# Optimization experiments

Hardware: AMD Instinct MI355X
Metric: run time of the kernel (lower is better)

The kernel has to match this reference:

```python
import jax, jax.numpy as jnp
import numpy as np

R = 32  # voxel resolution
B, CIN, COUT, N = 4, 64, 64, 4096
K = 3


def setup_inputs():
    key = jax.random.key(0)
    ks = jax.random.split(key, 8)
    s = 0.05
    return {
        "features": jax.random.normal(ks[0], (B, CIN, N), jnp.float32),
        "coords": jax.random.normal(ks[1], (B, 3, N), jnp.float32),
        # voxel branch: conv3d + BN x2
        "w1": jax.random.normal(ks[2], (COUT, CIN, K, K, K), jnp.float32) * s,
        "b1": jnp.zeros((COUT,), jnp.float32),
        "g1": jnp.ones((COUT,), jnp.float32),
        "be1": jnp.zeros((COUT,), jnp.float32),
        "w2": jax.random.normal(ks[3], (COUT, COUT, K, K, K), jnp.float32) * s,
        "b2": jnp.zeros((COUT,), jnp.float32),
        "g2": jnp.ones((COUT,), jnp.float32),
        "be2": jnp.zeros((COUT,), jnp.float32),
        # point branch SharedMLP (1x1 conv + BN + ReLU)
        "wp": jax.random.normal(ks[4], (COUT, CIN), jnp.float32) * s,
        "bp": jnp.zeros((COUT,), jnp.float32),
        "gp": jnp.ones((COUT,), jnp.float32),
        "bep": jnp.zeros((COUT,), jnp.float32),
        # fuzzy_proj 1x1 conv
        "wf": jax.random.normal(ks[5], (COUT, CIN), jnp.float32) * s,
        "bf": jnp.zeros((COUT,), jnp.float32),
        # fusion SharedMLP (3*COUT -> COUT)
        "wfu": jax.random.normal(ks[6], (COUT, 3 * COUT), jnp.float32) * s,
        "bfu": jnp.zeros((COUT,), jnp.float32),
        "gfu": jnp.ones((COUT,), jnp.float32),
        "befu": jnp.zeros((COUT,), jnp.float32),
    }


def _bn3d(x, g, b):
    # training-mode BatchNorm3d, eps=1e-4 (biased variance, as torch)
    m = x.mean((0, 2, 3, 4), keepdims=True)
    v = x.var((0, 2, 3, 4), keepdims=True)
    return (x - m) * jax.lax.rsqrt(v + 1e-4) * g[None, :, None, None, None] + b[None, :, None, None, None]


def _bn1d(x, g, b):
    m = x.mean((0, 2), keepdims=True)
    v = x.var((0, 2), keepdims=True)
    return (x - m) * jax.lax.rsqrt(v + 1e-4) * g[None, :, None] + b[None, :, None]


def _conv3d(x, w, b):
    pad = K // 2
    y = jax.lax.conv_general_dilated(x, w, (1, 1, 1), [(pad, pad)] * 3,
                                     dimension_numbers=('NCDHW', 'OIDHW', 'NCDHW'))
    return y + b[None, :, None, None, None]


def _conv1x1(x, w, b):
    return jnp.einsum('oc,bcn->bon', w, x) + b[None, :, None]


def _voxelize(features, coords):
    # PVCNN Voxelization(normalize=True, eps=0): center, scale to unit, grid coords in [0, R-1]
    nc = coords - coords.mean(axis=2, keepdims=True)              # [B,3,N]
    norm = jnp.linalg.norm(nc, axis=1, keepdims=True)             # [B,1,N]
    nc = nc / (norm.max(axis=2, keepdims=True) * 2.0) + 0.5
    nc = jnp.clip(nc * R, 0.0, R - 1)
    vox = jnp.round(nc).astype(jnp.int32)                         # [B,3,N]
    b_, c_, n_ = features.shape
    idx = (vox[:, 0] * R + vox[:, 1]) * R + vox[:, 2]             # [B,N]
    flat = (idx + jnp.arange(b_)[:, None] * R ** 3).reshape(-1)
    feat = features.transpose(0, 2, 1).reshape(b_ * n_, c_)
    sums = jax.ops.segment_sum(feat, flat, num_segments=b_ * R ** 3)
    cnt = jax.ops.segment_sum(jnp.ones((b_ * n_,), feat.dtype), flat, num_segments=b_ * R ** 3)
    avg = sums / jnp.maximum(cnt, 1.0)[:, None]                   # scatter-mean
    grid = avg.reshape(b_, R ** 3, c_).transpose(0, 2, 1).reshape(b_, c_, R, R, R)
    return grid, nc


def _devoxelize(grid, nc):
    # trilinear gather: grid [B,C,R,R,R], nc [B,3,N] float coords in [0,R-1]
    b_, c_ = grid.shape[:2]
    g = grid.reshape(b_, c_, -1)
    lo_f = jnp.floor(nc)
    fr = nc - lo_f                                                # fractional part [B,3,N]
    lo = lo_f.astype(jnp.int32)
    hi = jnp.minimum(lo + 1, R - 1)
    out = jnp.zeros((b_, c_, nc.shape[2]), grid.dtype)
    for dx in (0, 1):
        for dy in (0, 1):
            for dz in (0, 1):
                ix = hi[:, 0] if dx else lo[:, 0]
                iy = hi[:, 1] if dy else lo[:, 1]
                iz = hi[:, 2] if dz else lo[:, 2]
                w = ((fr[:, 0] if dx else 1.0 - fr[:, 0]) *
                     (fr[:, 1] if dy else 1.0 - fr[:, 1]) *
                     (fr[:, 2] if dz else 1.0 - fr[:, 2]))        # [B,N]
                flat = (ix * R + iy) * R + iz                     # [B,N]
                vals = jnp.take_along_axis(g, flat[:, None, :], axis=2)  # [B,C,N]
                out = out + vals * w[:, None, :]
    return out


def reference(features, coords, w1, b1, g1, be1, w2, b2, g2, be2,
              wp, bp, gp, bep, wf, bf, wfu, bfu, gfu, befu):
    lrelu = lambda x: jnp.where(x > 0, x, 0.1 * x)
    # voxel branch
    grid, nc = _voxelize(features, coords)
    v = lrelu(_bn3d(_conv3d(grid, w1, b1), g1, be1))
    v = lrelu(_bn3d(_conv3d(v, w2, b2), g2, be2))
    vox_feat = _devoxelize(v, nc)                                 # [B,COUT,N]
    # point branch
    pt = jax.nn.relu(_bn1d(_conv1x1(features, wp, bp), gp, bep))
    # fuzzy branch: dense attention over points
    cn = coords.transpose(0, 2, 1)                                # [B,N,3]
    cn = cn / jnp.maximum(jnp.linalg.norm(cn, axis=-1, keepdims=True), 1e-12)
    att = jax.nn.softmax(jnp.einsum('bnd,bmd->bnm', cn, cn) / 0.1, axis=-1)
    fz = jnp.einsum('bnm,bcm->bcn', att, features)                # [B,CIN,N]
    fz = _conv1x1(fz, wf, bf)
    # fusion
    comb = jnp.concatenate([vox_feat, pt, fz], axis=1)            # [B,3*COUT,N]
    fused = jax.nn.relu(_bn1d(_conv1x1(comb, wfu, bfu), gfu, befu))
    return (fused, coords)
```

## Files before the change

kernel.cpp:

```cpp
#include <hip/hip_runtime.h>
#include <hip/hip_bf16.h>
#include <math.h>

#define RR 32
#define R3 32768
#define BB 4
#define CI 64
#define CO 64
#define NN 4096

typedef short v8s __attribute__((ext_vector_type(8)));
typedef float v4f __attribute__((ext_vector_type(4)));
typedef unsigned short ushort_t;

__device__ __forceinline__ unsigned short f2bf(float f) {
    unsigned int u = __float_as_uint(f);
    unsigned int r = (u + 0x7FFFu + ((u >> 16) & 1u)) >> 16;
    return (unsigned short)r;
}

__device__ __forceinline__ void gll16(const void* g, void* l) {
    __builtin_amdgcn_global_load_lds((const __attribute__((address_space(1))) unsigned int*)g,
                                     (__attribute__((address_space(3))) unsigned int*)l, 16, 0, 0);
}

__device__ __forceinline__ float blockReduceSum(float v, float* sm) {
    int tid = threadIdx.x;
    sm[tid] = v; __syncthreads();
    for (int off = 128; off > 0; off >>= 1) {
        if (tid < off) sm[tid] += sm[tid + off];
        __syncthreads();
    }
    float r = sm[0]; __syncthreads();
    return r;
}
__device__ __forceinline__ float blockReduceMax(float v, float* sm) {
    int tid = threadIdx.x;
    sm[tid] = v; __syncthreads();
    for (int off = 128; off > 0; off >>= 1) {
        if (tid < off) sm[tid] = fmaxf(sm[tid], sm[tid + off]);
        __syncthreads();
    }
    float r = sm[0]; __syncthreads();
    return r;
}

__global__ void k_nc(const float* __restrict__ coords, float* __restrict__ nc,
                     int* __restrict__ vidx) {
    int b = blockIdx.x, tid = threadIdx.x;
    __shared__ float sm[256];
    const float* cb = coords + (size_t)b * 3 * NN;
    float s0 = 0, s1 = 0, s2 = 0;
    for (int n = tid; n < NN; n += 256) {
        s0 += cb[n]; s1 += cb[NN + n]; s2 += cb[2 * NN + n];
    }
    float m0 = blockReduceSum(s0, sm) * (1.0f / NN);
    float m1 = blockReduceSum(s1, sm) * (1.0f / NN);
    float m2 = blockReduceSum(s2, sm) * (1.0f / NN);
    float mx = 0;
    for (int n = tid; n < NN; n += 256) {
        float dx = cb[n] - m0, dy = cb[NN + n] - m1, dz = cb[2 * NN + n] - m2;
        mx = fmaxf(mx, dx * dx + dy * dy + dz * dz);
    }
    mx = blockReduceMax(mx, sm);
    float denom = 2.0f * sqrtf(mx);
    float mean[3] = {m0, m1, m2};
    for (int n = tid; n < NN; n += 256) {
        int vi[3];
        #pragma unroll
        for (int ax = 0; ax < 3; ax++) {
            float x = (cb[ax * NN + n] - mean[ax]) / denom + 0.5f;
            x = x * RR;
            x = fminf(fmaxf(x, 0.0f), (float)(RR - 1));
            nc[((size_t)b * 3 + ax) * NN + n] = x;
            vi[ax] = (int)rintf(x);
        }
        vidx[b * NN + n] = (vi[0] * RR + vi[1]) * RR + vi[2];
    }
}

__global__ void k_scatter(const float* __restrict__ feat, const int* __restrict__ vidx,
                          float* __restrict__ grid, float* __restrict__ cnt) {
    int i = blockIdx.x * 256 + threadIdx.x;
    int n = i & (NN - 1);
    int c = (i >> 12) & 63;
    int b = i >> 18;
    int idx = vidx[b * NN + n];
    atomicAdd(&grid[((size_t)(b * 64 + c)) * R3 + idx], feat[((size_t)(b * 64 + c)) * NN + n]);
    if (c == 0) atomicAdd(&cnt[b * R3 + idx], 1.0f);
}

__global__ void k_avgT(const float* __restrict__ grid, const float* __restrict__ cnt,
                       ushort_t* __restrict__ gT) {
    __shared__ float ld[64][65];
    int b = blockIdx.y, s0 = blockIdx.x * 64, tid = threadIdx.x;
    int sl = tid & 63, cq = tid >> 6;
    const float* xb = grid + (size_t)b * 64 * R3;
    #pragma unroll
    for (int k = 0; k < 16; k++) {
        int c = cq * 16 + k;
        ld[sl][c] = xb[(size_t)c * R3 + s0 + sl];
    }
    __syncthreads();
    int v = tid >> 2, q = tid & 3;
    float inv = 1.0f / fmaxf(cnt[b * R3 + s0 + v], 1.0f);
    unsigned int pk[8];
    #pragma unroll
    for (int j = 0; j < 8; j++) {
        int c = q * 16 + j * 2;
        float a = ld[v][c] * inv, d = ld[v][c + 1] * inv;
        pk[j] = (unsigned int)f2bf(a) | ((unsigned int)f2bf(d) << 16);
    }
    uint4* op = (uint4*)(gT + ((size_t)(b * R3 + s0 + v)) * 64 + q * 16);
    op[0] = make_uint4(pk[0], pk[1], pk[2], pk[3]);
    op[1] = make_uint4(pk[4], pk[5], pk[6], pk[7]);
}

__global__ void k_f2b(const float* __restrict__ x, ushort_t* __restrict__ o) {
    size_t i = (size_t)blockIdx.x * 256 + threadIdx.x;
    float4 a = ((const float4*)x)[i * 2];
    float4 b = ((const float4*)x)[i * 2 + 1];
    union { __hip_bfloat162 h[4]; uint4 u; } pk;
    pk.h[0] = __float22bfloat162_rn(make_float2(a.x, a.y));
    pk.h[1] = __float22bfloat162_rn(make_float2(a.z, a.w));
    pk.h[2] = __float22bfloat162_rn(make_float2(b.x, b.y));
    pk.h[3] = __float22bfloat162_rn(make_float2(b.z, b.w));
    ((uint4*)o)[i] = pk.u;
}

__global__ void k_tws(const float* __restrict__ w, ushort_t* __restrict__ wS) {
    int i = blockIdx.x * 256 + threadIdx.x;
    int cis = i & 31, co = (i >> 5) & 63;
    int dx = (i >> 11) % 3, cih = (i / 6144) & 1, dzdy = i / 12288;
    int k = dzdy * 3 + dx, ci = cih * 32 + cis;
    wS[i] = f2bf(w[((size_t)co * CI + ci) * 27 + k]);
}

__global__ void k_fold(const float* __restrict__ wp, const float* __restrict__ wfu,
                       const float* __restrict__ wf, const float* __restrict__ bf,
                       const float* __restrict__ bfu,
                       float* __restrict__ wpT, float* __restrict__ wfuT,
                       float* __restrict__ bC) {
    int i = blockIdx.x * 256 + threadIdx.x;
    if (i < 4096) {
        int c = i >> 6, o = i & 63;
        wpT[c * 64 + o] = wp[o * 64 + c];
    } else if (i < 12288) {
        int j = i - 4096;
        int c = j >> 6, o = j & 63;
        wfuT[c * 64 + o] = wfu[(size_t)o * 192 + c];
    } else if (i < 16384) {
        int j = i - 12288;
        int c = j >> 6, o = j & 63;
        float s = 0;
        for (int k = 0; k < 64; k++)
            s += wfu[(size_t)o * 192 + 128 + k] * wf[(size_t)k * 64 + c];
        wfuT[(128 + c) * 64 + o] = s;
    } else if (i < 16448) {
        int o = i - 16384;
        float s = bfu[o];
        for (int k = 0; k < 64; k++)
            s += wfu[(size_t)o * 192 + 128 + k] * bf[k];
        bC[o] = s;
    }
}

__global__ void k_bncast(const float* __restrict__ x, const float* __restrict__ accs,
                         const float* __restrict__ g, const float* __restrict__ be,
                         float invcnt, float slope, ushort_t* __restrict__ o) {
    size_t i = (size_t)blockIdx.x * 256 + threadIdx.x;
    int c0 = (int)((i * 8) & 63);
    float sc[8], sh[8];
    #pragma unroll
    for (int j = 0; j < 8; j++) {
        int c = c0 + j;
        float mean = accs[2 * c] * invcnt;
        float var = accs[2 * c + 1] * invcnt - mean * mean;
        float scale = g[c] * rsqrtf(var + 1e-4f);
        sc[j] = scale;
        sh[j] = be[c] - mean * scale;
    }
    float4 a = ((const float4*)x)[i * 2];
    float4 d = ((const float4*)x)[i * 2 + 1];
    float va[8] = {a.x, a.y, a.z, a.w, d.x, d.y, d.z, d.w};
    unsigned pk[4];
    #pragma unroll
    for (int j = 0; j < 4; j++) {
        float u0 = va[2 * j] * sc[2 * j] + sh[2 * j];
        float u1 = va[2 * j + 1] * sc[2 * j + 1] + sh[2 * j + 1];
        u0 = u0 > 0 ? u0 : slope * u0;
        u1 = u1 > 0 ? u1 : slope * u1;
        pk[j] = (unsigned)f2bf(u0) | ((unsigned)f2bf(u1) << 16);
    }
    ((uint4*)o)[i] = make_uint4(pk[0], pk[1], pk[2], pk[3]);
}

__global__ __launch_bounds__(256) void k_convlds(const ushort_t* __restrict__ gT,
                                                 const ushort_t* __restrict__ wS,
                                                 float* __restrict__ outCL,
                                                 float* __restrict__ accs) {
    __shared__ ushort_t lin[20480];
    __shared__ ushort_t lw[2][6144];
    int bid = blockIdx.x;
    int wgid = (bid & 7) * 64 + (bid >> 3);
    int yt = wgid & 3, z0 = (wgid >> 2) & 31, b = wgid >> 7;
    int tid = threadIdx.x;
    int w = __builtin_amdgcn_readfirstlane(tid >> 6);
    int lane = tid & 63, l15 = lane & 15, l4 = lane >> 4;
    int y0 = yt * 8;
    const ushort_t* gTb = gT + (size_t)b * R3 * 64;

    int voxF[4];
    #pragma unroll
    for (int f = 0; f < 4; f++)
        voxF[f] = (w * 2 + (f >> 1)) * 32 + (f & 1) * 16 + l15 - 1;
    bool xlo_ok = (l15 != 0), xhi_ok = (l15 != 15);

    const v8s vzero = {};
    v4f acc[4][4];
    #pragma unroll
    for (int m = 0; m < 4; m++)
        #pragma unroll
        for (int f = 0; f < 4; f++)
            acc[m][f] = (v4f){0.0f, 0.0f, 0.0f, 0.0f};

#define WSTAGE(s)                                                              \
    do {                                                                       \
        const ushort_t* _src = wS + (size_t)(s) * 6144;                        \
        ushort_t* _dst = lw[(s) & 1];                                          \
        _Pragma("unroll") for (int _i = 0; _i < 3; _i++) {                     \
            int _p = _i * 256 + w * 64;                                        \
            gll16(_src + (size_t)(_p + lane) * 8, _dst + (size_t)_p * 8);      \
        }                                                                      \
    } while (0)

#define ISTAGE(dz)                                                             \
    do {                                                                       \
        int _zp = z0 - 1 + (dz);                                               \
        if (_zp < 0 || _zp > 31) {                                             \
            for (int _q = 0; _q < 10; _q++)                                    \
                *(v8s*)&lin[(size_t)(w * 640 + _q * 64 + lane) * 8] = vzero;   \
        } else {                                                               \
            if (yt == 0) *(v8s*)&lin[(size_t)tid * 8] = vzero;                 \
            if (yt == 3) *(v8s*)&lin[(size_t)(2304 + tid) * 8] = vzero;        \
            const ushort_t* _pb = gTb + ((size_t)_zp * 1024 + (size_t)(y0 - 1) * 32) * 64; \
            int _g0 = (yt == 0) ? 256 : 0;                                     \
            int _nc = 10 - (yt == 0) - (yt == 3);                              \
            for (int _i = 0; _i < _nc; _i++) {                                 \
                int _pbase = _g0 + _i * 256 + w * 64;                          \
                int _p = _pbase + lane;                                        \
                int _vx = _p >> 3, _js = _p & 7;                               \
                int _sg = _vx * 8 + (_js ^ (_vx & 7));                         \
                gll16(_pb + (size_t)_sg * 8, lin + (size_t)_pbase * 8);        \
            }                                                                  \
        }                                                                      \
    } while (0)

    WSTAGE(0);
    for (int s = 0; s < 18; s++) {
        int dy = (s / 2) % 3, cih = s & 1;
        asm volatile("s_barrier" ::: "memory");
        if ((s % 6) == 0) ISTAGE(s / 6);
        if (s + 1 < 18) WSTAGE(s + 1);
        if (s + 1 < 18) asm volatile("s_waitcnt vmcnt(3) lgkmcnt(0)" ::: "memory");
        else            asm volatile("s_waitcnt vmcnt(0) lgkmcnt(0)" ::: "memory");
        asm volatile("s_barrier" ::: "memory");

        const ushort_t* lwb = lw[s & 1];
        #pragma unroll
        for (int dx = 0; dx < 3; dx++) {
            v8s Bf[4];
            #pragma unroll
            for (int f = 0; f < 4; f++) {
                int vox = voxF[f] + dy * 32 + dx;
                int g = vox * 8 + ((cih * 4 + l4) ^ (vox & 7));
                int bix = g * 16;
                bix = bix < 0 ? 0 : bix;
                v8s vb = *(const v8s*)((const char*)lin + bix);
                bool ok = (dx == 0 && (f & 1) == 0) ? xlo_ok :
                          (dx == 2 && (f & 1) == 1) ? xhi_ok : true;
                Bf[f] = ok ? vb : vzero;
            }
            const ushort_t* ap = lwb + dx * 2048 + l15 * 32 + l4 * 8;
            #pragma unroll
            for (int m = 0; m < 4; m++) {
                v8s Af = *(const v8s*)(ap + m * 512);
                #pragma unroll
                for (int f = 0; f < 4; f++)
                    acc[m][f] = __builtin_amdgcn_mfma_f32_16x16x32_bf16(Af, Bf[f], acc[m][f], 0, 0, 0);
            }
        }
    }

    #pragma unroll
    for (int m = 0; m < 4; m++) {
        #pragma unroll
        for (int f = 0; f < 4; f++) {
            int y = y0 + w * 2 + (f >> 1);
            int x = (f & 1) * 16 + l15;
            float4 o = make_float4(acc[m][f][0], acc[m][f][1], acc[m][f][2], acc[m][f][3]);
            *(float4*)&outCL[((size_t)b * R3 + z0 * 1024 + y * 32 + x) * 64 + m * 16 + l4 * 4] = o;
        }
    }

    __syncthreads();
    float* sbuf = (float*)lin;
    #pragma unroll
    for (int m = 0; m < 4; m++)
        #pragma unroll
        for (int r = 0; r < 4; r++) {
            float s = 0, q = 0;
            #pragma unroll
            for (int f = 0; f < 4; f++) {
                float v = acc[m][f][r];
                s += v; q += v * v;
            }
            sbuf[tid * 32 + (m * 4 + r) * 2] = s;
            sbuf[tid * 32 + (m * 4 + r) * 2 + 1] = q;
        }
    __syncthreads();
    if (tid < 128) {
        int co = tid >> 1, val = tid & 1;
        int m = co >> 4, cl4 = (co >> 2) & 3, r = co & 3;
        float a = 0;
        for (int w2 = 0; w2 < 4; w2++)
            for (int l = 0; l < 16; l++)
                a += sbuf[(w2 * 64 + cl4 * 16 + l) * 32 + (m * 4 + r) * 2 + val];
        atomicAdd(&accs[2 * co + val], a);
    }
#undef WSTAGE
#undef ISTAGE
}

__global__ void k_bnfin2(const float* __restrict__ pst, const float* __restrict__ g,
                         const float* __restrict__ be, float* __restrict__ stats,
                         float invcnt) {
    int c = blockIdx.x, tid = threadIdx.x;
    __shared__ float rs[256], rq[256];
    rs[tid] = pst[(c * 256 + tid) * 2];
    rq[tid] = pst[(c * 256 + tid) * 2 + 1];
    __syncthreads();
    for (int off = 128; off > 0; off >>= 1) {
        if (tid < off) { rs[tid] += rs[tid + off]; rq[tid] += rq[tid + off]; }
        __syncthreads();
    }
    if (tid == 0) {
        float mean = rs[0] * invcnt;
        float var = rq[0] * invcnt - mean * mean;
        float sc = g[c] * rsqrtf(var + 1e-4f);
        stats[2 * c] = sc;
        stats[2 * c + 1] = be[c] - mean * sc;
    }
}

__global__ void k_bn_act(const float* __restrict__ x, const float* __restrict__ stats,
                         float* __restrict__ out, int shift, float slope) {
    size_t i = (size_t)blockIdx.x * 256 + threadIdx.x;
    int c = (int)((i >> shift) & 63);
    float sc = stats[2 * c], sh = stats[2 * c + 1];
    float4 v = ((const float4*)x)[i];
    v.x = v.x * sc + sh; v.y = v.y * sc + sh; v.z = v.z * sc + sh; v.w = v.w * sc + sh;
    v.x = v.x > 0 ? v.x : slope * v.x;
    v.y = v.y > 0 ? v.y : slope * v.y;
    v.z = v.z > 0 ? v.z : slope * v.z;
    v.w = v.w > 0 ? v.w : slope * v.w;
    ((float4*)out)[i] = v;
}

__global__ void k_devox2(const float* __restrict__ gcl, const float* __restrict__ accs,
                         const float* __restrict__ g, const float* __restrict__ be,
                         float invcnt, const float* __restrict__ nc,
                         float* __restrict__ out) {
    int b = blockIdx.y;
    int tid = threadIdx.x, p = tid >> 4, q = tid & 15;
    int n = blockIdx.x * 16 + p;
    float x = nc[((size_t)b * 3 + 0) * NN + n];
    float y = nc[((size_t)b * 3 + 1) * NN + n];
    float z = nc[((size_t)b * 3 + 2) * NN + n];
    float fx = floorf(x), fy = floorf(y), fz = floorf(z);
    int lx = (int)fx, ly = (int)fy, lz = (int)fz;
    int hx = min(lx + 1, RR - 1), hy = min(ly + 1, RR - 1), hz = min(lz + 1, RR - 1);
    float frx = x - fx, fry = y - fy, frz = z - fz;
    int xx[2] = {lx, hx}, yy[2] = {ly, hy}, zz[2] = {lz, hz};
    float wx[2] = {1.0f - frx, frx}, wy[2] = {1.0f - fry, fry}, wz[2] = {1.0f - frz, frz};
    float sc[4], sh[4];
    #pragma unroll
    for (int j = 0; j < 4; j++) {
        int c = q * 4 + j;
        float mean = accs[2 * c] * invcnt;
        float var = accs[2 * c + 1] * invcnt - mean * mean;
        float scale = g[c] * rsqrtf(var + 1e-4f);
        sc[j] = scale;
        sh[j] = be[c] - mean * scale;
    }
    float a0 = 0, a1 = 0, a2 = 0, a3 = 0;
    #pragma unroll
    for (int dx = 0; dx < 2; dx++)
        #pragma unroll
        for (int dy = 0; dy < 2; dy++)
            #pragma unroll
            for (int dz = 0; dz < 2; dz++) {
                int idx = (xx[dx] * RR + yy[dy]) * RR + zz[dz];
                float wt = wx[dx] * wy[dy] * wz[dz];
                float4 v = *(const float4*)&gcl[((size_t)b * R3 + idx) * 64 + q * 4];
                float u0 = v.x * sc[0] + sh[0]; u0 = u0 > 0 ? u0 : 0.1f * u0;
                float u1 = v.y * sc[1] + sh[1]; u1 = u1 > 0 ? u1 : 0.1f * u1;
                float u2 = v.z * sc[2] + sh[2]; u2 = u2 > 0 ? u2 : 0.1f * u2;
                float u3 = v.w * sc[3] + sh[3]; u3 = u3 > 0 ? u3 : 0.1f * u3;
                a0 += wt * u0; a1 += wt * u1; a2 += wt * u2; a3 += wt * u3;
            }
    out[((size_t)(b * 64 + q * 4 + 0)) * NN + n] = a0;
    out[((size_t)(b * 64 + q * 4 + 1)) * NN + n] = a1;
    out[((size_t)(b * 64 + q * 4 + 2)) * NN + n] = a2;
    out[((size_t)(b * 64 + q * 4 + 3)) * NN + n] = a3;
}

__global__ __launch_bounds__(256) void k_fuzzym(const float* __restrict__ coords,
                                                const ushort_t* __restrict__ featb,
                                                float* __restrict__ pnum,
                                                float* __restrict__ pden) {
    __shared__ float cm[3][1024];
    __shared__ ushort_t la[2][2048];
    int b = blockIdx.z, mc = blockIdx.y, nt = blockIdx.x;
    int tid = threadIdx.x;
    int w = tid >> 6, lane = tid & 63, l15 = lane & 15, l4 = lane >> 4;
    int m0 = mc * 1024;

    for (int i = tid; i < 1024; i += 256) {
        float a0 = coords[((size_t)b * 3 + 0) * NN + m0 + i];
        float a1 = coords[((size_t)b * 3 + 1) * NN + m0 + i];
        float a2 = coords[((size_t)b * 3 + 2) * NN + m0 + i];
        float inv = 1.0f / fmaxf(sqrtf(a0 * a0 + a1 * a1 + a2 * a2), 1e-12f);
        cm[0][i] = a0 * inv; cm[1][i] = a1 * inv; cm[2][i] = a2 * inv;
    }

    int n = nt * 64 + w * 16 + l15;
    float q0 = coords[((size_t)b * 3 + 0) * NN + n];
    float q1 = coords[((size_t)b * 3 + 1) * NN + n];
    float q2 = coords[((size_t)b * 3 + 2) * NN + n];
    float qi = 10.0f / fmaxf(sqrtf(q0 * q0 + q1 * q1 + q2 * q2), 1e-12f);
    q0 *= qi; q1 *= qi; q2 *= qi;

    int srow = tid >> 2, sslot = tid & 3;
    int g0 = sslot ^ ((srow >> 1) & 3);
    const ushort_t* fb = featb + (size_t)b * 64 * NN + m0;
    const ushort_t* sbase = fb + (size_t)srow * NN + g0 * 8;
    int rsw = (l15 >> 1) & 3;

    v4f acc[4];
    #pragma unroll
    for (int cb = 0; cb < 4; cb++) acc[cb] = (v4f){0.0f, 0.0f, 0.0f, 0.0f};
    float den = 0.0f;

    gll16(sbase, &la[0][(size_t)tid * 8]);
    asm volatile("s_waitcnt vmcnt(0)" ::: "memory");
    __syncthreads();

    for (int t = 0; t < 32; t++) {
        int cur = t & 1;
        if (t + 1 < 32)
            gll16(sbase + (t + 1) * 32, &la[cur ^ 1][(size_t)tid * 8]);

        int mo = t * 32 + l4 * 8;
        float e[8];
        #pragma unroll
        for (int jj = 0; jj < 2; jj++) {
            float4 x0 = *(const float4*)&cm[0][mo + jj * 4];
            float4 x1 = *(const float4*)&cm[1][mo + jj * 4];
            float4 x2 = *(const float4*)&cm[2][mo + jj * 4];
            e[jj * 4 + 0] = __expf(q0 * x0.x + q1 * x1.x + q2 * x2.x);
            e[jj * 4 + 1] = __expf(q0 * x0.y + q1 * x1.y + q2 * x2.y);
            e[jj * 4 + 2] = __expf(q0 * x0.z + q1 * x1.z + q2 * x2.z);
            e[jj * 4 + 3] = __expf(q0 * x0.w + q1 * x1.w + q2 * x2.w);
        }
        den += ((e[0] + e[1]) + (e[2] + e[3])) + ((e[4] + e[5]) + (e[6] + e[7]));
        union { __hip_bfloat162 h[4]; v8s v; } pk;
        pk.h[0] = __float22bfloat162_rn(make_float2(e[0], e[1]));
        pk.h[1] = __float22bfloat162_rn(make_float2(e[2], e[3]));
        pk.h[2] = __float22bfloat162_rn(make_float2(e[4], e[5]));
        pk.h[3] = __float22bfloat162_rn(make_float2(e[6], e[7]));
        #pragma unroll
        for (int cb = 0; cb < 4; cb++) {
            v8s A = *(const v8s*)&la[cur][(size_t)((cb * 16 + l15) * 4 + (l4 ^ rsw)) * 8];
            acc[cb] = __builtin_amdgcn_mfma_f32_16x16x32_bf16(A, pk.v, acc[cb], 0, 0, 0);
        }
        asm volatile("s_waitcnt vmcnt(0)" ::: "memory");
        __syncthreads();
    }

    den += __shfl_xor(den, 16);
    den += __shfl_xor(den, 32);

    size_t obase = ((size_t)(b * 4 + mc)) * 64 * NN;
    #pragma unroll
    for (int cb = 0; cb < 4; cb++)
        #pragma unroll
        for (int r = 0; r < 4; r++)
            pnum[obase + (size_t)(cb * 16 + l4 * 4 + r) * NN + n] = acc[cb][r];
    if (l4 == 0) pden[((size_t)(b * 4 + mc)) * NN + n] = den;
}

__global__ void k_combine2(const float* __restrict__ pnum, const float* __restrict__ pden,
                           float* __restrict__ fzf) {
    int i = blockIdx.x * 256 + threadIdx.x;
    int b = i >> 18, c = (i >> 12) & 63, n = i & 4095;
    float num = 0, den = 0;
    #pragma unroll
    for (int ch = 0; ch < 4; ch++) {
        num += pnum[((size_t)(b * 4 + ch) * 64 + c) * NN + n];
        den += pden[((size_t)(b * 4 + ch)) * NN + n];
    }
    fzf[((size_t)(b * 64 + c)) * NN + n] = num / den;
}

__global__ __launch_bounds__(256) void k_1x1s(const float* __restrict__ in,
                                              const float* __restrict__ wT,
                                              const float* __restrict__ bias,
                                              float* __restrict__ out,
                                              float* __restrict__ pst) {
    int b = blockIdx.z, ob = blockIdx.y, bx = blockIdx.x;
    int tid = threadIdx.x;
    int q = tid & 15, o = ob * 16 + (tid >> 4);
    int n = bx * 64 + q * 4;
    const float* src = in + (size_t)b * 64 * NN + n;
    const float* wp_ = wT + o;
    v4f acc = {0, 0, 0, 0};
    #pragma unroll 8
    for (int c = 0; c < 64; c++) {
        float4 x = *(const float4*)&src[(size_t)c * NN];
        float w = wp_[c * 64];
        acc[0] += x.x * w; acc[1] += x.y * w; acc[2] += x.z * w; acc[3] += x.w * w;
    }
    float bv = bias[o];
    float s = 0, q2 = 0;
    float4 ov;
    float* op = (float*)&ov;
    #pragma unroll
    for (int v = 0; v < 4; v++) {
        float val = acc[v] + bv;
        op[v] = val;
        s += val; q2 += val * val;
    }
    *(float4*)&out[((size_t)(b * 64 + o)) * NN + n] = ov;
    #pragma unroll
    for (int off = 1; off < 16; off <<= 1) {
        s += __shfl_xor(s, off);
        q2 += __shfl_xor(q2, off);
    }
    if (q == 0) {
        int part = bx * 4 + b;
        pst[(o * 256 + part) * 2] = s;
        pst[(o * 256 + part) * 2 + 1] = q2;
    }
}

__global__ __launch_bounds__(256) void k_1x1f(const float* __restrict__ vox,
                                              const float* __restrict__ pt,
                                              const float* __restrict__ fzf,
                                              const float* __restrict__ bnB,
                                              const float* __restrict__ wfuT,
                                              const float* __restrict__ bC,
                                              float* __restrict__ out,
                                              float* __restrict__ pst) {
    int b = blockIdx.z, ob = blockIdx.y, bx = blockIdx.x;
    int tid = threadIdx.x;
    int q = tid & 15, o = ob * 16 + (tid >> 4);
    int n = bx * 64 + q * 4;
    const float* srcA = vox + (size_t)b * 64 * NN + n;
    const float* srcB = pt + (size_t)b * 64 * NN + n;
    const float* srcC = fzf + (size_t)b * 64 * NN + n;
    const float* wA = wfuT + o;
    v4f acc = {0, 0, 0, 0};
    #pragma unroll 8
    for (int c = 0; c < 64; c++) {
        float4 x = *(const float4*)&srcA[(size_t)c * NN];
        float w = wA[c * 64];
        acc[0] += x.x * w; acc[1] += x.y * w; acc[2] += x.z * w; acc[3] += x.w * w;
    }
    #pragma unroll 8
    for (int c = 0; c < 64; c++) {
        float4 x = *(const float4*)&srcB[(size_t)c * NN];
        float sc = bnB[2 * c], sh = bnB[2 * c + 1];
        float w = wA[(64 + c) * 64];
        float x0 = fmaxf(x.x * sc + sh, 0.0f), x1 = fmaxf(x.y * sc + sh, 0.0f);
        float x2 = fmaxf(x.z * sc + sh, 0.0f), x3 = fmaxf(x.w * sc + sh, 0.0f);
        acc[0] += x0 * w; acc[1] += x1 * w; acc[2] += x2 * w; acc[3] += x3 * w;
    }
    #pragma unroll 8
    for (int c = 0; c < 64; c++) {
        float4 x = *(const float4*)&srcC[(size_t)c * NN];
        float w = wA[(128 + c) * 64];
        acc[0] += x.x * w; acc[1] += x.y * w; acc[2] += x.z * w; acc[3] += x.w * w;
    }
    float bv = bC[o];
    float s = 0, q2 = 0;
    float4 ov;
    float* op = (float*)&ov;
    #pragma unroll
    for (int v = 0; v < 4; v++) {
        float val = acc[v] + bv;
        op[v] = val;
        s += val; q2 += val * val;
    }
    *(float4*)&out[((size_t)(b * 64 + o)) * NN + n] = ov;
    #pragma unroll
    for (int off = 1; off < 16; off <<= 1) {
        s += __shfl_xor(s, off);
        q2 += __shfl_xor(q2, off);
    }
    if (q == 0) {
        int part = bx * 4 + b;
        pst[(o * 256 + part) * 2] = s;
        pst[(o * 256 + part) * 2 + 1] = q2;
    }
}

extern "C" void kernel_launch(void* const* d_in, const int* in_sizes, int n_in,
                              void* d_out, int out_size, void* d_ws, size_t ws_size,
                              hipStream_t stream) {
    const float* features = (const float*)d_in[0];
    const float* coords = (const float*)d_in[1];
    const float* w1 = (const float*)d_in[2];
    const float* g1 = (const float*)d_in[4];
    const float* be1 = (const float*)d_in[5];
    const float* w2 = (const float*)d_in[6];
    const float* g2 = (const float*)d_in[8];
    const float* be2 = (const float*)d_in[9];
    const float* wp = (const float*)d_in[10];
    const float* bp = (const float*)d_in[11];
    const float* gp = (const float*)d_in[12];
    const float* bep = (const float*)d_in[13];
    const float* wf = (const float*)d_in[14];
    const float* bf = (const float*)d_in[15];
    const float* wfu = (const float*)d_in[16];
    const float* bfu = (const float*)d_in[17];
    const float* gfu = (const float*)d_in[18];
    const float* befu = (const float*)d_in[19];

    float* ws = (float*)d_ws;
    float* nc = ws;
    int* vidx = (int*)(ws + 49152);
    float* cnt = ws + 65536;
    float* pden = cnt;
    float* gridA = ws + 196608;
    float* gridCL = gridA;
    float* gTpool = ws + 8585216;
    ushort_t* gT = (ushort_t*)gTpool;
    float* pnum = gTpool;
    float* pstB = gTpool;
    float* stats = ws + 16973824;
    float* voxreg = ws + 16974336;
    ushort_t* wS1 = (ushort_t*)voxreg;
    ushort_t* wS2 = wS1 + 110592;
    float* vox = voxreg;
    float* pt = ws + 18022912;
    float* fzf = ws + 19071488;
    float* wpT = ws + 20120064;
    float* wfuT = wpT + 4096;
    float* bC = wfuT + 12288;
    float* fpre = ws + 21168640;
    ushort_t* featb = (ushort_t*)fpre;
    float* accs = ws + 22217216;

    float* out = (float*)d_out;

    hipMemsetAsync(accs, 0, 512 * 4, stream);
    hipMemsetAsync(cnt, 0, (size_t)(131072 + 8388608) * 4, stream);

    k_fold<<<65, 256, 0, stream>>>(wp, wfu, wf, bf, bfu, wpT, wfuT, bC);
    k_f2b<<<BB * 64 * NN / 8 / 256, 256, 0, stream>>>(features, featb);
    k_tws<<<432, 256, 0, stream>>>(w1, wS1);
    k_tws<<<432, 256, 0, stream>>>(w2, wS2);
    k_nc<<<BB, 256, 0, stream>>>(coords, nc, vidx);
    k_scatter<<<BB * 64 * NN / 256, 256, 0, stream>>>(features, vidx, gridA, cnt);
    k_avgT<<<dim3(512, BB), 256, 0, stream>>>(gridA, cnt, gT);

    k_convlds<<<512, 256, 0, stream>>>(gT, wS1, gridCL, accs);
    k_bncast<<<BB * R3 * 64 / 8 / 256, 256, 0, stream>>>(gridCL, accs, g1, be1,
                                                         1.0f / (BB * R3), 0.1f, gT);
    k_convlds<<<512, 256, 0, stream>>>(gT, wS2, gridCL, accs + 128);
    k_devox2<<<dim3(NN / 16, BB), 256, 0, stream>>>(gridCL, accs + 128, g2, be2,
                                                    1.0f / (BB * R3), nc, vox);

    k_fuzzym<<<dim3(64, 4, BB), 256, 0, stream>>>(coords, featb, pnum, pden);
    k_combine2<<<BB * 64 * NN / 256, 256, 0, stream>>>(pnum, pden, fzf);

    k_1x1s<<<dim3(NN / 64, 4, BB), 256, 0, stream>>>(features, wpT, bp, pt, pstB);
    k_bnfin2<<<64, 256, 0, stream>>>(pstB, gp, bep, stats + 256, 1.0f / (BB * NN));

    k_1x1f<<<dim3(NN / 64, 4, BB), 256, 0, stream>>>(vox, pt, fzf, stats + 256, wfuT, bC,
                                                     fpre, pstB);
    k_bnfin2<<<64, 256, 0, stream>>>(pstB, gfu, befu, stats + 384, 1.0f / (BB * NN));
    k_bn_act<<<BB * 64 * NN / 4 / 256, 256, 0, stream>>>(fpre, stats + 384, out, 10, 0.0f);

    hipMemcpyAsync(out + (size_t)BB * CO * NN, coords, (size_t)BB * 3 * NN * 4,
                   hipMemcpyDeviceToDevice, stream);
}
```

Before: 287.9 us.

## Replace atomic voxel scatter with counting-sort bucket lists and gather

Voxelization no longer scatters every feature channel into a dense fp32 grid with atomics and then averages and transposes it. Instead it counts points per voxel, builds per-voxel point lists with a prefix scan and fill pass, transposes the features to channel-last, and has one wave per voxel gather and average its points straight into the bf16 channel-last grid. This removes the large memset of the fp32 grid, the per-channel atomics and the separate average/transpose pass. In exchange it adds several small launches (scan, fill, transpose) and data-dependent per-voxel loops with serial index lookups.

```diff
diff --git a/kernel.cpp b/kernel.cpp
--- a/kernel.cpp
+++ b/kernel.cpp
@@ -46,7 +46,7 @@
 }
 
 __global__ void k_nc(const float* __restrict__ coords, float* __restrict__ nc,
-                     int* __restrict__ vidx) {
+                     int* __restrict__ vidx, int* __restrict__ cntI) {
     int b = blockIdx.x, tid = threadIdx.x;
     __shared__ float sm[256];
     const float* cb = coords + (size_t)b * 3 * NN;
@@ -75,45 +75,93 @@
             nc[((size_t)b * 3 + ax) * NN + n] = x;
             vi[ax] = (int)rintf(x);
         }
-        vidx[b * NN + n] = (vi[0] * RR + vi[1]) * RR + vi[2];
-    }
-}
-
-__global__ void k_scatter(const float* __restrict__ feat, const int* __restrict__ vidx,
-                          float* __restrict__ grid, float* __restrict__ cnt) {
+        int idx = (vi[0] * RR + vi[1]) * RR + vi[2];
+        vidx[b * NN + n] = idx;
+        atomicAdd(&cntI[b * R3 + idx], 1);
+    }
+}
+
+__global__ void k_scan1(const int* __restrict__ cntI, int* __restrict__ lscan,
+                        int* __restrict__ bsum) {
+    __shared__ int sm[256];
+    int tid = threadIdx.x;
+    int i = blockIdx.x * 256 + tid;
+    int v = cntI[i];
+    sm[tid] = v; __syncthreads();
+    for (int off = 1; off < 256; off <<= 1) {
+        int t = (tid >= off) ? sm[tid - off] : 0;
+        __syncthreads();
+        sm[tid] += t;
+        __syncthreads();
+    }
+    lscan[i] = sm[tid] - v;
+    if (tid == 255) bsum[blockIdx.x] = sm[tid];
+}
+
+__global__ void k_scan2(const int* __restrict__ bsum, int* __restrict__ bbase) {
+    __shared__ int sm[512];
+    int tid = threadIdx.x;
+    int v = bsum[tid];
+    sm[tid] = v; __syncthreads();
+    for (int off = 1; off < 512; off <<= 1) {
+        int t = (tid >= off) ? sm[tid - off] : 0;
+        __syncthreads();
+        sm[tid] += t;
+        __syncthreads();
+    }
+    bbase[tid] = sm[tid] - v;
+}
+
+__global__ void k_fill(const int* __restrict__ vidx, const int* __restrict__ lscan,
+                       const int* __restrict__ bbase, int* __restrict__ rank,
+                       int* __restrict__ plist) {
     int i = blockIdx.x * 256 + threadIdx.x;
-    int n = i & (NN - 1);
-    int c = (i >> 12) & 63;
-    int b = i >> 18;
-    int idx = vidx[b * NN + n];
-    atomicAdd(&grid[((size_t)(b * 64 + c)) * R3 + idx], feat[((size_t)(b * 64 + c)) * NN + n]);
-    if (c == 0) atomicAdd(&cnt[b * R3 + idx], 1.0f);
-}
-
-__global__ void k_avgT(const float* __restrict__ grid, const float* __restrict__ cnt,
-                       ushort_t* __restrict__ gT) {
-    __shared__ float ld[64][65];
-    int b = blockIdx.y, s0 = blockIdx.x * 64, tid = threadIdx.x;
-    int sl = tid & 63, cq = tid >> 6;
-    const float* xb = grid + (size_t)b * 64 * R3;
+    int b = i >> 12, n = i & (NN - 1);
+    int flat = b * R3 + vidx[i];
+    int r = atomicAdd(&rank[flat], 1);
+    plist[bbase[flat >> 8] + lscan[flat] + r] = n;
+}
+
+__global__ void k_tfcl(const float* __restrict__ feat, float* __restrict__ featT) {
+    __shared__ float t[64][65];
+    int b = blockIdx.y, n0 = blockIdx.x * 64, tid = threadIdx.x;
+    int q = tid >> 6, nl = tid & 63;
     #pragma unroll
     for (int k = 0; k < 16; k++) {
-        int c = cq * 16 + k;
-        ld[sl][c] = xb[(size_t)c * R3 + s0 + sl];
+        int c = q * 16 + k;
+        t[nl][c] = feat[((size_t)(b * CI + c)) * NN + n0 + nl];
     }
     __syncthreads();
-    int v = tid >> 2, q = tid & 3;
-    float inv = 1.0f / fmaxf(cnt[b * R3 + s0 + v], 1.0f);
-    unsigned int pk[8];
-    #pragma unroll
-    for (int j = 0; j < 8; j++) {
-        int c = q * 16 + j * 2;
-        float a = ld[v][c] * inv, d = ld[v][c + 1] * inv;
-        pk[j] = (unsigned int)f2bf(a) | ((unsigned int)f2bf(d) << 16);
-    }
-    uint4* op = (uint4*)(gT + ((size_t)(b * R3 + s0 + v)) * 64 + q * 16);
-    op[0] = make_uint4(pk[0], pk[1], pk[2], pk[3]);
-    op[1] = make_uint4(pk[4], pk[5], pk[6], pk[7]);
+    #pragma unroll
+    for (int k = 0; k < 16; k++) {
+        int n = q * 16 + k;
+        featT[((size_t)b * NN + n0 + n) * 64 + nl] = t[n][nl];
+    }
+}
+
+__global__ __launch_bounds__(256) void k_gather(const float* __restrict__ featT,
+                                                const int* __restrict__ cntI,
+                                                const int* __restrict__ lscan,
+                                                const int* __restrict__ bbase,
+                                                const int* __restrict__ plist,
+                                                ushort_t* __restrict__ gT) {
+    int wv = threadIdx.x >> 6, lane = threadIdx.x & 63;
+    int vbase = blockIdx.x * 32 + wv * 8;
+    for (int k = 0; k < 8; k++) {
+        int flat = vbase + k;
+        int count = cntI[flat];
+        float s = 0.0f;
+        if (count > 0) {
+            int b = flat >> 15;
+            int start = bbase[flat >> 8] + lscan[flat];
+            for (int j = 0; j < count; j++) {
+                int n = plist[start + j];
+                s += featT[((size_t)b * NN + n) * 64 + lane];
+            }
+            s *= 1.0f / (float)count;
+        }
+        gT[(size_t)flat * 64 + lane] = f2bf(s);
+    }
 }
 
 __global__ void k_f2b(const float* __restrict__ x, ushort_t* __restrict__ o) {
@@ -640,10 +688,15 @@
     float* ws = (float*)d_ws;
     float* nc = ws;
     int* vidx = (int*)(ws + 49152);
-    float* cnt = ws + 65536;
-    float* pden = cnt;
-    float* gridA = ws + 196608;
-    float* gridCL = gridA;
+    int* cntI = (int*)(ws + 65536);
+    float* pden = ws + 65536;
+    float* gridCL = ws + 196608;
+    int* lscan = (int*)(ws + 196608);
+    int* bsum = (int*)(ws + 327680);
+    int* bbase = (int*)(ws + 328192);
+    int* rank = (int*)(ws + 328704);
+    int* plist = (int*)(ws + 459776);
+    float* featT = ws + 476160;
     float* gTpool = ws + 8585216;
     ushort_t* gT = (ushort_t*)gTpool;
     float* pnum = gTpool;
@@ -665,15 +718,20 @@
     float* out = (float*)d_out;
 
     hipMemsetAsync(accs, 0, 512 * 4, stream);
-    hipMemsetAsync(cnt, 0, (size_t)(131072 + 8388608) * 4, stream);
+    hipMemsetAsync(cntI, 0, 131072 * 4, stream);
+    hipMemsetAsync(rank, 0, 131072 * 4, stream);
 
     k_fold<<<65, 256, 0, stream>>>(wp, wfu, wf, bf, bfu, wpT, wfuT, bC);
     k_f2b<<<BB * 64 * NN / 8 / 256, 256, 0, stream>>>(features, featb);
     k_tws<<<432, 256, 0, stream>>>(w1, wS1);
     k_tws<<<432, 256, 0, stream>>>(w2, wS2);
-    k_nc<<<BB, 256, 0, stream>>>(coords, nc, vidx);
-    k_scatter<<<BB * 64 * NN / 256, 256, 0, stream>>>(features, vidx, gridA, cnt);
-    k_avgT<<<dim3(512, BB), 256, 0, stream>>>(gridA, cnt, gT);
+    k_tfcl<<<dim3(64, BB), 256, 0, stream>>>(features, featT);
+
+    k_nc<<<BB, 256, 0, stream>>>(coords, nc, vidx, cntI);
+    k_scan1<<<512, 256, 0, stream>>>(cntI, lscan, bsum);
+    k_scan2<<<1, 512, 0, stream>>>(bsum, bbase);
+    k_fill<<<BB * NN / 256, 256, 0, stream>>>(vidx, lscan, bbase, rank, plist);
+    k_gather<<<4096, 256, 0, stream>>>(featT, cntI, lscan, bbase, plist, gT);
 
     k_convlds<<<512, 256, 0, stream>>>(gT, wS1, gridCL, accs);
     k_bncast<<<BB * R3 * 64 / 8 / 256, 256, 0, stream>>>(gridCL, accs, g1, be1,
```

New measurement: 275.1 us. 4.4% less time.
